# Optimization experiments

Measured on AMD Instinct MI355X. Metric: run time of the kernel, lower is better.

Reference implementation:

```python
import jax, jax.numpy as jnp
import numpy as np

B, S, D = 8, 2048, 512
EPS = 1e-6
ROPE_THETA = 10000.0


def setup_inputs() -> dict:
    key = jax.random.key(0)
    ks = jax.random.split(key, 8)
    scale = 0.02
    return {
        "x": jax.random.normal(ks[0], (B, S, D), dtype=jnp.float32),
        "conv_w": jax.random.normal(ks[1], (D, D, 3), dtype=jnp.float32) * scale,
        "conv_b": jnp.zeros((D,), dtype=jnp.float32),
        "pre_g": jnp.ones((D,), dtype=jnp.float32),
        "q_g": jnp.ones((D,), dtype=jnp.float32),
        "k_g": jnp.ones((D,), dtype=jnp.float32),
        "Wq": jax.random.normal(ks[2], (D, D), dtype=jnp.float32) * scale,
        "Wk": jax.random.normal(ks[3], (D, D), dtype=jnp.float32) * scale,
        "Wv": jax.random.normal(ks[4], (D, D), dtype=jnp.float32) * scale,
    }


def _rmsnorm(x, g, eps=EPS):
    ms = jnp.mean(jnp.square(x), axis=-1, keepdims=True)
    return x * jax.lax.rsqrt(ms + eps) * g


def _rope_tables(seq_len, head_dim, dtype=jnp.float32):
    inv = 1.0 / (ROPE_THETA ** (jnp.arange(0, head_dim, 2, dtype=dtype) / head_dim))
    freqs = jnp.arange(seq_len, dtype=dtype)[:, None] * inv[None, :]  # [S, D/2]
    return jnp.cos(freqs), jnp.sin(freqs)


def _apply_rope(x, cos, sin):
    # x: [B, S, D]; treat last dim as D/2 complex pairs (interleaved real/imag)
    b, s, d = x.shape
    xr = x.reshape(b, s, d // 2, 2)
    x0, x1 = xr[..., 0], xr[..., 1]
    c = cos[None, :, :]
    sn = sin[None, :, :]
    o0 = x0 * c - x1 * sn
    o1 = x0 * sn + x1 * c
    return jnp.stack([o0, o1], axis=-1).reshape(b, s, d)


def reference(x, conv_w, conv_b, pre_g, q_g, k_g, Wq, Wk, Wv):
    b, s, d = x.shape
    # Conv1d over sequence axis (kernel 3, padding 1)
    xc = jnp.transpose(x, (0, 2, 1))  # [B, D, S]
    xc = jax.lax.conv_general_dilated(
        xc, conv_w, window_strides=(1,), padding=[(1, 1)],
        dimension_numbers=("NCH", "OIH", "NCH"))
    xc = xc + conv_b[None, :, None]
    x_norm = _rmsnorm(jnp.transpose(xc, (0, 2, 1)), pre_g)  # [B, S, D]

    q = _rmsnorm(jnp.einsum("bsd,ed->bse", x_norm, Wq), q_g)
    k = _rmsnorm(jnp.einsum("bsd,ed->bse", x_norm, Wk), k_g)
    v = jnp.einsum("bsd,ed->bse", x_norm, Wv)

    cos, sin = _rope_tables(s, d, x.dtype)
    q = _apply_rope(q, cos, sin)
    k = _apply_rope(k, cos, sin)

    scores = jnp.einsum("bqd,bkd->bqk", q, k) / jnp.sqrt(jnp.asarray(d, x.dtype))
    w = jax.nn.softmax(scores, axis=-1)  # dropout is identity in eval mode
    attended = jnp.einsum("bqk,bkd->bqd", w, v)
    out = x + attended
    return out.mean(axis=1)  # [B, D]
```

## Files before the change

### kernel.cpp

```cpp
#include <hip/hip_runtime.h>
#include <math.h>

#define BB 8
#define SS 2048
#define SSG 2050
#define DDIM 512
#define KC 1536
#define EPSV 1e-6f
#define SCALE 0.044194173824159216f

typedef unsigned short ushort_t;
using short8 = __attribute__((ext_vector_type(8))) short;
using f32x4  = __attribute__((ext_vector_type(4))) float;

__device__ inline unsigned short f2bf(float f) {
    union { float f; unsigned int u; } v; v.f = f;
    unsigned int r = v.u + 0x7FFFu + ((v.u >> 16) & 1u);
    return (unsigned short)(r >> 16);
}
__device__ inline unsigned int packbf(float a, float b) {
    return (unsigned int)f2bf(a) | ((unsigned int)f2bf(b) << 16);
}
__device__ inline float bf2f(unsigned short s) {
    union { unsigned int u; float f; } v; v.u = ((unsigned int)s) << 16; return v.f;
}

__device__ inline void gload16(const ushort_t* g, ushort_t* l) {
    __builtin_amdgcn_global_load_lds(
        (__attribute__((address_space(1))) const void*)g,
        (__attribute__((address_space(3))) void*)l, 16, 0, 0);
}

__device__ inline short8 ldswz(const ushort_t* s, int row, int c) {
    return *reinterpret_cast<const short8*>(&s[(row << 6) + ((c ^ (row & 7)) << 3)]);
}

__global__ __launch_bounds__(256) void kx_cast(const float* __restrict__ x,
                                               ushort_t* __restrict__ xbf,
                                               float* __restrict__ xsum)
{
    const int t = threadIdx.x;
    const int b = blockIdx.y;
    const int r0 = blockIdx.x * 16;
    const int c0 = 2 * t;
    if (blockIdx.x == 0) {
        *reinterpret_cast<unsigned int*>(&xbf[((size_t)b * SSG) * DDIM + c0]) = 0u;
        *reinterpret_cast<unsigned int*>(&xbf[((size_t)b * SSG + SS + 1) * DDIM + c0]) = 0u;
    }
    float s0 = 0.f, s1 = 0.f;
    for (int r = 0; r < 16; r++) {
        size_t srow = (size_t)b * SS + r0 + r;
        size_t drow = (size_t)b * SSG + 1 + r0 + r;
        float2 v = *reinterpret_cast<const float2*>(&x[srow * DDIM + c0]);
        s0 += v.x; s1 += v.y;
        *reinterpret_cast<unsigned int*>(&xbf[drow * DDIM + c0]) = packbf(v.x, v.y);
    }
    atomicAdd(&xsum[b * DDIM + c0], s0);
    atomicAdd(&xsum[b * DDIM + c0 + 1], s1);
}

__global__ __launch_bounds__(256) void k0_prep(
    const float* __restrict__ conv_w, const float* __restrict__ Wq,
    const float* __restrict__ Wk, const float* __restrict__ Wv,
    ushort_t* __restrict__ wcat, ushort_t* __restrict__ wqkv)
{
    int idx = blockIdx.x * 256 + threadIdx.x;
    {
        int o = idx / KC, kk = idx - o * KC;
        int t = kk >> 9, i = kk & 511;
        wcat[idx] = f2bf(conv_w[(size_t)o * KC + i * 3 + t]);
    }
    {
        int n = idx >> 9, d = idx & 511;
        const float* src = (n < 512) ? &Wq[(size_t)n * DDIM + d]
                         : (n < 1024) ? &Wk[(size_t)(n - 512) * DDIM + d]
                         : &Wv[(size_t)(n - 1024) * DDIM + d];
        wqkv[idx] = f2bf(*src);
    }
}

#define COMPUTE_TILE(Acur, Bcur) do { \
    _Pragma("unroll") \
    for (int half = 0; half < 2; half++) { \
        const int cb = (half << 2) | lq; \
        short8 af0 = ldswz(Acur, wm * 64 +  0 + lm, cb); \
        short8 af1 = ldswz(Acur, wm * 64 + 16 + lm, cb); \
        short8 af2 = ldswz(Acur, wm * 64 + 32 + lm, cb); \
        short8 af3 = ldswz(Acur, wm * 64 + 48 + lm, cb); \
        _Pragma("unroll") \
        for (int nt = 0; nt < 4; nt++) { \
            short8 bfv = ldswz(Bcur, wn * 64 + nt * 16 + lm, cb); \
            acc[0][nt] = __builtin_amdgcn_mfma_f32_16x16x32_bf16(af0, bfv, acc[0][nt], 0, 0, 0); \
            acc[1][nt] = __builtin_amdgcn_mfma_f32_16x16x32_bf16(af1, bfv, acc[1][nt], 0, 0, 0); \
            acc[2][nt] = __builtin_amdgcn_mfma_f32_16x16x32_bf16(af2, bfv, acc[2][nt], 0, 0, 0); \
            acc[3][nt] = __builtin_amdgcn_mfma_f32_16x16x32_bf16(af3, bfv, acc[3][nt], 0, 0, 0); \
        } \
    } } while (0)

__global__ __launch_bounds__(256) void k1b_conv(
    const ushort_t* __restrict__ xbf, const ushort_t* __restrict__ wcat,
    const float* __restrict__ conv_b, ushort_t* __restrict__ ybf, float* __restrict__ rs)
{
    __shared__ alignas(16) ushort_t As[2][128 * 64];
    __shared__ alignas(16) ushort_t Bs[2][128 * 64];
    const int t = threadIdx.x;
    const int lane = t & 63, w = t >> 6;
    const int lm = lane & 15, lq = lane >> 4;
    const int wm = w >> 1, wn = w & 1;
    const int lr = lane >> 3;
    const int lc = ((lane & 7) ^ lr) << 3;
    const int s0 = blockIdx.x * 128;
    const int n0 = blockIdx.y * 128;
    const int b  = blockIdx.z;
    const ushort_t* Ag = xbf + (size_t)b * SSG * DDIM;
    const ushort_t* Bg = wcat + (size_t)n0 * KC;

    const ushort_t* pa[4]; const ushort_t* pb[4];
    int la[4];
    #pragma unroll
    for (int i = 0; i < 4; i++) {
        const int tr = (w * 4 + i) * 8 + lr;
        pa[i] = &Ag[(size_t)(s0 + tr) * DDIM + lc];
        pb[i] = &Bg[(size_t)tr * KC + lc];
        la[i] = (w * 4 + i) * 512;
    }

    f32x4 acc[4][4];
    #pragma unroll
    for (int i = 0; i < 4; i++)
        #pragma unroll
        for (int j = 0; j < 4; j++) acc[i][j] = (f32x4){0.f, 0.f, 0.f, 0.f};

    #define STG1B(tn, bufi) do { \
        const int koA = (tn) * 64; \
        _Pragma("unroll") \
        for (int i = 0; i < 4; i++) { \
            gload16(pa[i] + koA, &As[bufi][la[i]]); \
            gload16(pb[i] + koA, &Bs[bufi][la[i]]); \
        } } while (0)

    const int NT = 24;
    STG1B(0, 0);
    __syncthreads();
    for (int dc = 0; dc < NT; dc++) {
        const int cur = dc & 1;
        if (dc + 1 < NT) STG1B(dc + 1, cur ^ 1);
        COMPUTE_TILE(&As[cur][0], &Bs[cur][0]);
        __syncthreads();
    }
    #undef STG1B

    const int rbase = s0 + wm * 64;
    const int cbase = n0 + wn * 64;
    ushort_t* yb = ybf + (size_t)b * SS * DDIM;
    float* rsb = rs + (size_t)b * SS;
    float bias[4];
    #pragma unroll
    for (int nt = 0; nt < 4; nt++) bias[nt] = conv_b[cbase + nt * 16 + lm];
    #pragma unroll
    for (int mt = 0; mt < 4; mt++) {
        float pr[4] = {0.f, 0.f, 0.f, 0.f};
        #pragma unroll
        for (int nt = 0; nt < 4; nt++) {
            #pragma unroll
            for (int r = 0; r < 4; r++) {
                float val = acc[mt][nt][r] + bias[nt];
                yb[(size_t)(rbase + mt * 16 + lq * 4 + r) * DDIM + cbase + nt * 16 + lm] = f2bf(val);
                pr[r] = fmaf(val, val, pr[r]);
            }
        }
        #pragma unroll
        for (int r = 0; r < 4; r++) {
            float p = pr[r];
            p += __shfl_xor(p, 1, 64); p += __shfl_xor(p, 2, 64);
            p += __shfl_xor(p, 4, 64); p += __shfl_xor(p, 8, 64);
            if (lm == 0) atomicAdd(&rsb[rbase + mt * 16 + lq * 4 + r], p);
        }
    }
}

__global__ __launch_bounds__(256) void k1n_norm(
    const ushort_t* __restrict__ ybf, const float* __restrict__ rs,
    const float* __restrict__ pre_g, ushort_t* __restrict__ xnbf)
{
    const int t = threadIdx.x;
    const int b = blockIdx.y;
    const int r0 = blockIdx.x * 8;
    float2 pg = *reinterpret_cast<const float2*>(&pre_g[2 * t]);
    for (int r = 0; r < 8; r++) {
        size_t row = (size_t)b * SS + r0 + r;
        float inv = rsqrtf(rs[row] * (1.0f / DDIM) + EPSV);
        unsigned int yv = *reinterpret_cast<const unsigned int*>(&ybf[row * DDIM + 2 * t]);
        float v0 = bf2f((ushort_t)(yv & 0xFFFF)), v1 = bf2f((ushort_t)(yv >> 16));
        *reinterpret_cast<unsigned int*>(&xnbf[row * DDIM + 2 * t]) =
            packbf(v0 * inv * pg.x, v1 * inv * pg.y);
    }
}

__global__ __launch_bounds__(256) void k1c_qkv(
    const ushort_t* __restrict__ xnbf, const ushort_t* __restrict__ wqkv,
    ushort_t* __restrict__ qraw, ushort_t* __restrict__ kraw, ushort_t* __restrict__ vb,
    float* __restrict__ rq, float* __restrict__ rk)
{
    __shared__ alignas(16) ushort_t As[2][128 * 64];
    __shared__ alignas(16) ushort_t Bs[2][128 * 64];
    const int t = threadIdx.x;
    const int lane = t & 63, w = t >> 6;
    const int lm = lane & 15, lq = lane >> 4;
    const int wm = w >> 1, wn = w & 1;
    const int lr = lane >> 3;
    const int lc = ((lane & 7) ^ lr) << 3;
    const int s0 = blockIdx.x * 128;
    const int n0 = blockIdx.y * 128;
    const int b  = blockIdx.z;
    const ushort_t* Ag = xnbf + ((size_t)b * SS + s0) * DDIM;
    const ushort_t* Bg = wqkv + (size_t)n0 * DDIM;

    const ushort_t* pa[4]; const ushort_t* pb[4];
    int la[4];
    #pragma unroll
    for (int i = 0; i < 4; i++) {
        const int tr = (w * 4 + i) * 8 + lr;
        pa[i] = &Ag[(size_t)tr * DDIM + lc];
        pb[i] = &Bg[(size_t)tr * DDIM + lc];
        la[i] = (w * 4 + i) * 512;
    }

    f32x4 acc[4][4];
    #pragma unroll
    for (int i = 0; i < 4; i++)
        #pragma unroll
        for (int j = 0; j < 4; j++) acc[i][j] = (f32x4){0.f, 0.f, 0.f, 0.f};

    #define STG1C(tn, bufi) do { \
        const int ko = (tn) * 64; \
        _Pragma("unroll") \
        for (int i = 0; i < 4; i++) { \
            gload16(pa[i] + ko, &As[bufi][la[i]]); \
            gload16(pb[i] + ko, &Bs[bufi][la[i]]); \
        } } while (0)

    const int NT = 8;
    STG1C(0, 0);
    __syncthreads();
    for (int dc = 0; dc < NT; dc++) {
        const int cur = dc & 1;
        if (dc + 1 < NT) STG1C(dc + 1, cur ^ 1);
        COMPUTE_TILE(&As[cur][0], &Bs[cur][0]);
        __syncthreads();
    }
    #undef STG1C

    const int which = blockIdx.y >> 2;
    const int rbase = s0 + wm * 64;
    const int cbase = ((blockIdx.y & 3) * 128) + wn * 64;
    if (which == 2) {
        ushort_t* vbb = vb + (size_t)b * SS * DDIM;
        #pragma unroll
        for (int mt = 0; mt < 4; mt++)
            #pragma unroll
            for (int nt = 0; nt < 4; nt++)
                #pragma unroll
                for (int r = 0; r < 4; r++)
                    vbb[(size_t)(rbase + mt * 16 + lq * 4 + r) * DDIM + cbase + nt * 16 + lm] =
                        f2bf(acc[mt][nt][r]);
    } else {
        ushort_t* db2 = (which ? kraw : qraw) + (size_t)b * SS * DDIM;
        float* rb = (which ? rk : rq) + (size_t)b * SS;
        #pragma unroll
        for (int mt = 0; mt < 4; mt++) {
            float pr[4] = {0.f, 0.f, 0.f, 0.f};
            #pragma unroll
            for (int nt = 0; nt < 4; nt++) {
                #pragma unroll
                for (int r = 0; r < 4; r++) {
                    float val = acc[mt][nt][r];
                    db2[(size_t)(rbase + mt * 16 + lq * 4 + r) * DDIM + cbase + nt * 16 + lm] = f2bf(val);
                    pr[r] = fmaf(val, val, pr[r]);
                }
            }
            #pragma unroll
            for (int r = 0; r < 4; r++) {
                float p = pr[r];
                p += __shfl_xor(p, 1, 64); p += __shfl_xor(p, 2, 64);
                p += __shfl_xor(p, 4, 64); p += __shfl_xor(p, 8, 64);
                if (lm == 0) atomicAdd(&rb[rbase + mt * 16 + lq * 4 + r], p);
            }
        }
    }
}

__global__ __launch_bounds__(256) void k1d_rope(
    ushort_t* q_io, ushort_t* k_io,
    const float* __restrict__ rq, const float* __restrict__ rk,
    const float* __restrict__ q_g, const float* __restrict__ k_g)
{
    const int t = threadIdx.x;
    const int b = blockIdx.y;
    const int r0 = blockIdx.x * 8;
    const int c0 = 2 * t;
    float qg0 = q_g[c0], qg1 = q_g[c0 + 1];
    float kg0 = k_g[c0], kg1 = k_g[c0 + 1];
    float invf = (float)pow(10000.0, -(double)c0 / (double)DDIM);
    for (int r = 0; r < 8; r++) {
        int srow = r0 + r;
        size_t rowi = (size_t)b * SS + srow;
        float iq = rsqrtf(rq[rowi] * (1.0f / DDIM) + EPSV);
        float ik = rsqrtf(rk[rowi] * (1.0f / DDIM) + EPSV);
        size_t off = rowi * DDIM + c0;
        unsigned int qv = *reinterpret_cast<const unsigned int*>(&q_io[off]);
        unsigned int kv = *reinterpret_cast<const unsigned int*>(&k_io[off]);
        float q0 = bf2f((ushort_t)(qv & 0xFFFF)) * iq * qg0;
        float q1 = bf2f((ushort_t)(qv >> 16)) * iq * qg1;
        float k0v = bf2f((ushort_t)(kv & 0xFFFF)) * ik * kg0;
        float k1v = bf2f((ushort_t)(kv >> 16)) * ik * kg1;
        float ang = (float)srow * invf, sn, cs;
        sincosf(ang, &sn, &cs);
        *reinterpret_cast<unsigned int*>(&q_io[off]) = packbf(q0 * cs - q1 * sn, q0 * sn + q1 * cs);
        *reinterpret_cast<unsigned int*>(&k_io[off]) = packbf(k0v * cs - k1v * sn, k0v * sn + k1v * cs);
    }
}

__global__ __launch_bounds__(256) void k2a_rowsum(
    const ushort_t* __restrict__ qb, const ushort_t* __restrict__ kb,
    ushort_t* __restrict__ P, float* __restrict__ l)
{
    __shared__ alignas(16) ushort_t As[2][128 * 64];
    __shared__ alignas(16) ushort_t Bs[2][128 * 64];
    const int t = threadIdx.x;
    const int lane = t & 63, w = t >> 6;
    const int lm = lane & 15, lq = lane >> 4;
    const int wm = w >> 1, wn = w & 1;
    const int lr = lane >> 3;
    const int lc = ((lane & 7) ^ lr) << 3;
    const int b  = blockIdx.x;
    const int qt = blockIdx.y;
    const int kt = blockIdx.z;
    const ushort_t* Ag = qb + ((size_t)b * SS + qt * 128) * DDIM;
    const ushort_t* Bg = kb + ((size_t)b * SS + kt * 128) * DDIM;

    const ushort_t* pa[4]; const ushort_t* pb[4];
    int la[4];
    #pragma unroll
    for (int i = 0; i < 4; i++) {
        const int tr = (w * 4 + i) * 8 + lr;
        pa[i] = &Ag[(size_t)tr * DDIM + lc];
        pb[i] = &Bg[(size_t)tr * DDIM + lc];
        la[i] = (w * 4 + i) * 512;
    }

    f32x4 acc[4][4];
    #pragma unroll
    for (int i = 0; i < 4; i++)
        #pragma unroll
        for (int j = 0; j < 4; j++) acc[i][j] = (f32x4){0.f, 0.f, 0.f, 0.f};

    #define STG2A(tn, bufi) do { \
        const int ko = (tn) * 64; \
        _Pragma("unroll") \
        for (int i = 0; i < 4; i++) { \
            gload16(pa[i] + ko, &As[bufi][la[i]]); \
            gload16(pb[i] + ko, &Bs[bufi][la[i]]); \
        } } while (0)

    const int NT = 8;
    STG2A(0, 0);
    __syncthreads();
    for (int dc = 0; dc < NT; dc++) {
        const int cur = dc & 1;
        if (dc + 1 < NT) STG2A(dc + 1, cur ^ 1);
        COMPUTE_TILE(&As[cur][0], &Bs[cur][0]);
        __syncthreads();
    }
    #undef STG2A

    const int rbase = qt * 128 + wm * 64;
    const int cbase = kt * 128 + wn * 64;
    ushort_t* Pb = P + (size_t)b * SS * SS;
    float* lrow = l + (size_t)b * SS;
    #pragma unroll
    for (int mt = 0; mt < 4; mt++) {
        #pragma unroll
        for (int r = 0; r < 4; r++) {
            const int row = rbase + mt * 16 + lq * 4 + r;
            float rowp = 0.f;
            #pragma unroll
            for (int nt = 0; nt < 4; nt++) {
                float e = __expf(acc[mt][nt][r] * SCALE);
                Pb[(size_t)row * SS + cbase + nt * 16 + lm] = f2bf(e);
                rowp += e;
            }
            float p = rowp;
            p += __shfl_xor(p, 1, 64); p += __shfl_xor(p, 2, 64);
            p += __shfl_xor(p, 4, 64); p += __shfl_xor(p, 8, 64);
            if (lm == 0) atomicAdd(&lrow[row], p);
        }
    }
}

__global__ __launch_bounds__(256) void k2c_colred(
    const ushort_t* __restrict__ P, const float* __restrict__ l,
    float* __restrict__ cw)
{
    const int t = threadIdx.x;
    const int b = blockIdx.z;
    const int k0 = blockIdx.x * 1024 + t * 4;
    const int q0 = blockIdx.y * 128;
    const ushort_t* Pb = P + ((size_t)b * SS + q0) * SS;
    const float* lb = l + (size_t)b * SS + q0;
    float a0 = 0.f, a1 = 0.f, a2 = 0.f, a3 = 0.f;
    for (int q = 0; q < 128; q++) {
        float rl = 1.0f / lb[q];
        uint2 pp = *reinterpret_cast<const uint2*>(&Pb[(size_t)q * SS + k0]);
        a0 = fmaf(bf2f((ushort_t)(pp.x & 0xFFFF)), rl, a0);
        a1 = fmaf(bf2f((ushort_t)(pp.x >> 16)), rl, a1);
        a2 = fmaf(bf2f((ushort_t)(pp.y & 0xFFFF)), rl, a2);
        a3 = fmaf(bf2f((ushort_t)(pp.y >> 16)), rl, a3);
    }
    atomicAdd(&cw[(size_t)b * SS + k0], a0);
    atomicAdd(&cw[(size_t)b * SS + k0 + 1], a1);
    atomicAdd(&cw[(size_t)b * SS + k0 + 2], a2);
    atomicAdd(&cw[(size_t)b * SS + k0 + 3], a3);
}

__global__ __launch_bounds__(256) void k4_out(
    const float* __restrict__ xsum, const ushort_t* __restrict__ v,
    const float* __restrict__ cwv, float* __restrict__ out)
{
    const int b = blockIdx.x, c = blockIdx.y;
    const int t = threadIdx.x;
    const int srow0 = c * (SS / 16);
    const ushort_t* vb = v + ((size_t)b * SS + srow0) * DDIM;
    const float* cwb   = cwv + (size_t)b * SS + srow0;
    float a0 = (c == 0) ? xsum[b * DDIM + t]       : 0.f;
    float a1 = (c == 0) ? xsum[b * DDIM + t + 256] : 0.f;
    for (int r = 0; r < SS / 16; r++) {
        float w = cwb[r];
        a0 += w * bf2f(vb[(size_t)r * DDIM + t]);
        a1 += w * bf2f(vb[(size_t)r * DDIM + t + 256]);
    }
    atomicAdd(&out[b * DDIM + t],       a0 * (1.0f / SS));
    atomicAdd(&out[b * DDIM + t + 256], a1 * (1.0f / SS));
}

extern "C" void kernel_launch(void* const* d_in, const int* in_sizes, int n_in,
                              void* d_out, int out_size, void* d_ws, size_t ws_size,
                              hipStream_t stream)
{
    const float* x      = (const float*)d_in[0];
    const float* conv_w = (const float*)d_in[1];
    const float* conv_b = (const float*)d_in[2];
    const float* pre_g  = (const float*)d_in[3];
    const float* q_g    = (const float*)d_in[4];
    const float* k_g    = (const float*)d_in[5];
    const float* Wq     = (const float*)d_in[6];
    const float* Wk     = (const float*)d_in[7];
    const float* Wv     = (const float*)d_in[8];
    float* out          = (float*)d_out;

    const size_t NTOK  = (size_t)BB * SS * DDIM;
    const size_t NTOKG = (size_t)BB * SSG * DDIM;
    char* p = (char*)d_ws;
    ushort_t* xbf = (ushort_t*)p; p += NTOKG * 2;
    ushort_t* ybf = (ushort_t*)p; p += NTOK * 2;
    ushort_t* xn  = (ushort_t*)p; p += NTOK * 2;
                         p += NTOK * 2;
    ushort_t* qio = (ushort_t*)p; p += NTOK * 2;
    ushort_t* kio = (ushort_t*)p; p += NTOK * 2;
    ushort_t* vb  = (ushort_t*)p; p += NTOK * 2;
    ushort_t* wcat = (ushort_t*)p; p += (size_t)DDIM * KC * 2;
    ushort_t* wqkv = (ushort_t*)p; p += (size_t)KC * DDIM * 2;
    float* rs   = (float*)p; p += (size_t)BB * SS * 4;
    float* rq   = (float*)p; p += (size_t)BB * SS * 4;
    float* rk   = (float*)p; p += (size_t)BB * SS * 4;
    float* lbuf = (float*)p; p += (size_t)BB * SS * 4;
    float* cwb  = (float*)p; p += (size_t)BB * SS * 4;
    float* xsum = (float*)p; p += (size_t)BB * DDIM * 4;

    ushort_t* Pbuf = xbf;

    (void)hipMemsetAsync(d_out, 0, (size_t)out_size * sizeof(float), stream);
    (void)hipMemsetAsync(rs, 0, ((size_t)BB * SS * 5 + (size_t)BB * DDIM) * sizeof(float), stream);

    kx_cast<<<dim3(SS / 16, BB), 256, 0, stream>>>(x, xbf, xsum);
    k0_prep<<<dim3(DDIM * KC / 256), 256, 0, stream>>>(conv_w, Wq, Wk, Wv, wcat, wqkv);
    k1b_conv<<<dim3(SS / 128, 4, BB), 256, 0, stream>>>(xbf, wcat, conv_b, ybf, rs);
    k1n_norm<<<dim3(SS / 8, BB), 256, 0, stream>>>(ybf, rs, pre_g, xn);
    k1c_qkv<<<dim3(SS / 128, 12, BB), 256, 0, stream>>>(xn, wqkv, qio, kio, vb, rq, rk);
    k1d_rope<<<dim3(SS / 8, BB), 256, 0, stream>>>(qio, kio, rq, rk, q_g, k_g);
    k2a_rowsum<<<dim3(BB, SS / 128, SS / 128), 256, 0, stream>>>(qio, kio, Pbuf, lbuf);
    k2c_colred<<<dim3(SS / 1024, SS / 128, BB), 256, 0, stream>>>(Pbuf, lbuf, cwb);
    k4_out<<<dim3(BB, 16), 256, 0, stream>>>(xsum, vb, cwb, out);
}
```

Measured before the change: 284.0 us.

## Halve GEMM K-tile to 32 with new swizzled LDS layout and precompute RoPE table

```diff
diff --git a/kernel.cpp b/kernel.cpp
--- a/kernel.cpp
+++ b/kernel.cpp
@@ -31,8 +31,10 @@
         (__attribute__((address_space(3))) void*)l, 16, 0, 0);
 }
 
-__device__ inline short8 ldswz(const ushort_t* s, int row, int c) {
-    return *reinterpret_cast<const short8*>(&s[(row << 6) + ((c ^ (row & 7)) << 3)]);
+__device__ inline short8 ldtile(const ushort_t* base, int R, int c) {
+    const int v = R >> 1;
+    const int s = (((c << 1) | (R & 1)) ^ (v & 7));
+    return *reinterpret_cast<const short8*>(&base[v * 64 + s * 8]);
 }
 
 __global__ __launch_bounds__(256) void kx_cast(const float* __restrict__ x,
@@ -79,51 +81,65 @@
     }
 }
 
-#define COMPUTE_TILE(Acur, Bcur) do { \
+__global__ __launch_bounds__(256) void ktab(float* __restrict__ rope)
+{
+    const int t = threadIdx.x;
+    const int r0 = blockIdx.x * 8;
+    const float invf = (float)pow(10000.0, -(double)(2 * t) / (double)DDIM);
+    for (int r = 0; r < 8; r++) {
+        int srow = r0 + r;
+        float sn, cs;
+        sincosf((float)srow * invf, &sn, &cs);
+        *reinterpret_cast<float2*>(&rope[((size_t)srow << 9) + 2 * t]) = make_float2(cs, sn);
+    }
+}
+
+#define COMPUTE_TILE32(Acur, Bcur) do { \
+    short8 av[4], bv[4]; \
     _Pragma("unroll") \
-    for (int half = 0; half < 2; half++) { \
-        const int cb = (half << 2) | lq; \
-        short8 af0 = ldswz(Acur, wm * 64 +  0 + lm, cb); \
-        short8 af1 = ldswz(Acur, wm * 64 + 16 + lm, cb); \
-        short8 af2 = ldswz(Acur, wm * 64 + 32 + lm, cb); \
-        short8 af3 = ldswz(Acur, wm * 64 + 48 + lm, cb); \
+    for (int mt = 0; mt < 4; mt++) av[mt] = ldtile(Acur, wm * 64 + mt * 16 + lm, lq); \
+    _Pragma("unroll") \
+    for (int nt = 0; nt < 4; nt++) bv[nt] = ldtile(Bcur, wn * 64 + nt * 16 + lm, lq); \
+    _Pragma("unroll") \
+    for (int nt = 0; nt < 4; nt++) { \
+        acc[0][nt] = __builtin_amdgcn_mfma_f32_16x16x32_bf16(av[0], bv[nt], acc[0][nt], 0, 0, 0); \
+        acc[1][nt] = __builtin_amdgcn_mfma_f32_16x16x32_bf16(av[1], bv[nt], acc[1][nt], 0, 0, 0); \
+        acc[2][nt] = __builtin_amdgcn_mfma_f32_16x16x32_bf16(av[2], bv[nt], acc[2][nt], 0, 0, 0); \
+        acc[3][nt] = __builtin_amdgcn_mfma_f32_16x16x32_bf16(av[3], bv[nt], acc[3][nt], 0, 0, 0); \
+    } } while (0)
+
+#define STAGE_PTRS(PA, GBASE, PITCH) \
+    { \
         _Pragma("unroll") \
-        for (int nt = 0; nt < 4; nt++) { \
-            short8 bfv = ldswz(Bcur, wn * 64 + nt * 16 + lm, cb); \
-            acc[0][nt] = __builtin_amdgcn_mfma_f32_16x16x32_bf16(af0, bfv, acc[0][nt], 0, 0, 0); \
-            acc[1][nt] = __builtin_amdgcn_mfma_f32_16x16x32_bf16(af1, bfv, acc[1][nt], 0, 0, 0); \
-            acc[2][nt] = __builtin_amdgcn_mfma_f32_16x16x32_bf16(af2, bfv, acc[2][nt], 0, 0, 0); \
-            acc[3][nt] = __builtin_amdgcn_mfma_f32_16x16x32_bf16(af3, bfv, acc[3][nt], 0, 0, 0); \
+        for (int rd = 0; rd < 2; rd++) { \
+            int v = rd * 32 + (t >> 3); \
+            int u = (t & 7) ^ (v & 7); \
+            int lrow = 2 * v + (u & 1); \
+            int chunk = u >> 1; \
+            PA[rd] = &GBASE[(size_t)lrow * (PITCH) + chunk * 8]; \
         } \
-    } } while (0)
+    }
 
 __global__ __launch_bounds__(256) void k1b_conv(
     const ushort_t* __restrict__ xbf, const ushort_t* __restrict__ wcat,
     const float* __restrict__ conv_b, ushort_t* __restrict__ ybf, float* __restrict__ rs)
 {
-    __shared__ alignas(16) ushort_t As[2][128 * 64];
-    __shared__ alignas(16) ushort_t Bs[2][128 * 64];
+    __shared__ alignas(16) ushort_t As[2][4096];
+    __shared__ alignas(16) ushort_t Bs[2][4096];
     const int t = threadIdx.x;
     const int lane = t & 63, w = t >> 6;
     const int lm = lane & 15, lq = lane >> 4;
     const int wm = w >> 1, wn = w & 1;
-    const int lr = lane >> 3;
-    const int lc = ((lane & 7) ^ lr) << 3;
     const int s0 = blockIdx.x * 128;
     const int n0 = blockIdx.y * 128;
     const int b  = blockIdx.z;
-    const ushort_t* Ag = xbf + (size_t)b * SSG * DDIM;
+    const ushort_t* Ag = xbf + ((size_t)b * SSG + s0) * DDIM;
     const ushort_t* Bg = wcat + (size_t)n0 * KC;
 
-    const ushort_t* pa[4]; const ushort_t* pb[4];
-    int la[4];
-    #pragma unroll
-    for (int i = 0; i < 4; i++) {
-        const int tr = (w * 4 + i) * 8 + lr;
-        pa[i] = &Ag[(size_t)(s0 + tr) * DDIM + lc];
-        pb[i] = &Bg[(size_t)tr * KC + lc];
-        la[i] = (w * 4 + i) * 512;
-    }
+    const ushort_t* pa[2]; const ushort_t* pb[2];
+    STAGE_PTRS(pa, Ag, DDIM);
+    STAGE_PTRS(pb, Bg, KC);
+    const int wb = w * 512;
 
     f32x4 acc[4][4];
     #pragma unroll
@@ -131,21 +147,19 @@
         #pragma unroll
         for (int j = 0; j < 4; j++) acc[i][j] = (f32x4){0.f, 0.f, 0.f, 0.f};
 
-    #define STG1B(tn, bufi) do { \
-        const int koA = (tn) * 64; \
-        _Pragma("unroll") \
-        for (int i = 0; i < 4; i++) { \
-            gload16(pa[i] + koA, &As[bufi][la[i]]); \
-            gload16(pb[i] + koA, &Bs[bufi][la[i]]); \
-        } } while (0)
-
-    const int NT = 24;
+    #define STG1B(tn, bufi) do { const int ko = (tn) * 32; \
+        gload16(pa[0] + ko, &As[bufi][wb]); \
+        gload16(pa[1] + ko, &As[bufi][2048 + wb]); \
+        gload16(pb[0] + ko, &Bs[bufi][wb]); \
+        gload16(pb[1] + ko, &Bs[bufi][2048 + wb]); } while (0)
+
+    const int NT = 48;
     STG1B(0, 0);
     __syncthreads();
     for (int dc = 0; dc < NT; dc++) {
         const int cur = dc & 1;
         if (dc + 1 < NT) STG1B(dc + 1, cur ^ 1);
-        COMPUTE_TILE(&As[cur][0], &Bs[cur][0]);
+        COMPUTE_TILE32(&As[cur][0], &Bs[cur][0]);
         __syncthreads();
     }
     #undef STG1B
@@ -202,29 +216,22 @@
     ushort_t* __restrict__ qraw, ushort_t* __restrict__ kraw, ushort_t* __restrict__ vb,
     float* __restrict__ rq, float* __restrict__ rk)
 {
-    __shared__ alignas(16) ushort_t As[2][128 * 64];
-    __shared__ alignas(16) ushort_t Bs[2][128 * 64];
+    __shared__ alignas(16) ushort_t As[2][4096];
+    __shared__ alignas(16) ushort_t Bs[2][4096];
     const int t = threadIdx.x;
     const int lane = t & 63, w = t >> 6;
     const int lm = lane & 15, lq = lane >> 4;
     const int wm = w >> 1, wn = w & 1;
-    const int lr = lane >> 3;
-    const int lc = ((lane & 7) ^ lr) << 3;
     const int s0 = blockIdx.x * 128;
     const int n0 = blockIdx.y * 128;
     const int b  = blockIdx.z;
     const ushort_t* Ag = xnbf + ((size_t)b * SS + s0) * DDIM;
     const ushort_t* Bg = wqkv + (size_t)n0 * DDIM;
 
-    const ushort_t* pa[4]; const ushort_t* pb[4];
-    int la[4];
-    #pragma unroll
-    for (int i = 0; i < 4; i++) {
-        const int tr = (w * 4 + i) * 8 + lr;
-        pa[i] = &Ag[(size_t)tr * DDIM + lc];
-        pb[i] = &Bg[(size_t)tr * DDIM + lc];
-        la[i] = (w * 4 + i) * 512;
-    }
+    const ushort_t* pa[2]; const ushort_t* pb[2];
+    STAGE_PTRS(pa, Ag, DDIM);
+    STAGE_PTRS(pb, Bg, DDIM);
+    const int wb = w * 512;
 
     f32x4 acc[4][4];
     #pragma unroll
@@ -232,21 +239,19 @@
         #pragma unroll
         for (int j = 0; j < 4; j++) acc[i][j] = (f32x4){0.f, 0.f, 0.f, 0.f};
 
-    #define STG1C(tn, bufi) do { \
-        const int ko = (tn) * 64; \
-        _Pragma("unroll") \
-        for (int i = 0; i < 4; i++) { \
-            gload16(pa[i] + ko, &As[bufi][la[i]]); \
-            gload16(pb[i] + ko, &Bs[bufi][la[i]]); \
-        } } while (0)
-
-    const int NT = 8;
+    #define STG1C(tn, bufi) do { const int ko = (tn) * 32; \
+        gload16(pa[0] + ko, &As[bufi][wb]); \
+        gload16(pa[1] + ko, &As[bufi][2048 + wb]); \
+        gload16(pb[0] + ko, &Bs[bufi][wb]); \
+        gload16(pb[1] + ko, &Bs[bufi][2048 + wb]); } while (0)
+
+    const int NT = 16;
     STG1C(0, 0);
     __syncthreads();
     for (int dc = 0; dc < NT; dc++) {
         const int cur = dc & 1;
         if (dc + 1 < NT) STG1C(dc + 1, cur ^ 1);
-        COMPUTE_TILE(&As[cur][0], &Bs[cur][0]);
+        COMPUTE_TILE32(&As[cur][0], &Bs[cur][0]);
         __syncthreads();
     }
     #undef STG1C
@@ -293,7 +298,8 @@
 __global__ __launch_bounds__(256) void k1d_rope(
     ushort_t* q_io, ushort_t* k_io,
     const float* __restrict__ rq, const float* __restrict__ rk,
-    const float* __restrict__ q_g, const float* __restrict__ k_g)
+    const float* __restrict__ q_g, const float* __restrict__ k_g,
+    const float* __restrict__ rope)
 {
     const int t = threadIdx.x;
     const int b = blockIdx.y;
@@ -301,7 +307,6 @@
     const int c0 = 2 * t;
     float qg0 = q_g[c0], qg1 = q_g[c0 + 1];
     float kg0 = k_g[c0], kg1 = k_g[c0 + 1];
-    float invf = (float)pow(10000.0, -(double)c0 / (double)DDIM);
     for (int r = 0; r < 8; r++) {
         int srow = r0 + r;
         size_t rowi = (size_t)b * SS + srow;
@@ -314,8 +319,8 @@
         float q1 = bf2f((ushort_t)(qv >> 16)) * iq * qg1;
         float k0v = bf2f((ushort_t)(kv & 0xFFFF)) * ik * kg0;
         float k1v = bf2f((ushort_t)(kv >> 16)) * ik * kg1;
-        float ang = (float)srow * invf, sn, cs;
-        sincosf(ang, &sn, &cs);
+        float2 cs2 = *reinterpret_cast<const float2*>(&rope[((size_t)srow << 9) + c0]);
+        float cs = cs2.x, sn = cs2.y;
         *reinterpret_cast<unsigned int*>(&q_io[off]) = packbf(q0 * cs - q1 * sn, q0 * sn + q1 * cs);
         *reinterpret_cast<unsigned int*>(&k_io[off]) = packbf(k0v * cs - k1v * sn, k0v * sn + k1v * cs);
     }
@@ -325,29 +330,22 @@
     const ushort_t* __restrict__ qb, const ushort_t* __restrict__ kb,
     ushort_t* __restrict__ P, float* __restrict__ l)
 {
-    __shared__ alignas(16) ushort_t As[2][128 * 64];
-    __shared__ alignas(16) ushort_t Bs[2][128 * 64];
+    __shared__ alignas(16) ushort_t As[2][4096];
+    __shared__ alignas(16) ushort_t Bs[2][4096];
     const int t = threadIdx.x;
     const int lane = t & 63, w = t >> 6;
     const int lm = lane & 15, lq = lane >> 4;
     const int wm = w >> 1, wn = w & 1;
-    const int lr = lane >> 3;
-    const int lc = ((lane & 7) ^ lr) << 3;
     const int b  = blockIdx.x;
     const int qt = blockIdx.y;
     const int kt = blockIdx.z;
     const ushort_t* Ag = qb + ((size_t)b * SS + qt * 128) * DDIM;
     const ushort_t* Bg = kb + ((size_t)b * SS + kt * 128) * DDIM;
 
-    const ushort_t* pa[4]; const ushort_t* pb[4];
-    int la[4];
-    #pragma unroll
-    for (int i = 0; i < 4; i++) {
-        const int tr = (w * 4 + i) * 8 + lr;
-        pa[i] = &Ag[(size_t)tr * DDIM + lc];
-        pb[i] = &Bg[(size_t)tr * DDIM + lc];
-        la[i] = (w * 4 + i) * 512;
-    }
+    const ushort_t* pa[2]; const ushort_t* pb[2];
+    STAGE_PTRS(pa, Ag, DDIM);
+    STAGE_PTRS(pb, Bg, DDIM);
+    const int wb = w * 512;
 
     f32x4 acc[4][4];
     #pragma unroll
@@ -355,21 +353,19 @@
         #pragma unroll
         for (int j = 0; j < 4; j++) acc[i][j] = (f32x4){0.f, 0.f, 0.f, 0.f};
 
-    #define STG2A(tn, bufi) do { \
-        const int ko = (tn) * 64; \
-        _Pragma("unroll") \
-        for (int i = 0; i < 4; i++) { \
-            gload16(pa[i] + ko, &As[bufi][la[i]]); \
-            gload16(pb[i] + ko, &Bs[bufi][la[i]]); \
-        } } while (0)
-
-    const int NT = 8;
+    #define STG2A(tn, bufi) do { const int ko = (tn) * 32; \
+        gload16(pa[0] + ko, &As[bufi][wb]); \
+        gload16(pa[1] + ko, &As[bufi][2048 + wb]); \
+        gload16(pb[0] + ko, &Bs[bufi][wb]); \
+        gload16(pb[1] + ko, &Bs[bufi][2048 + wb]); } while (0)
+
+    const int NT = 16;
     STG2A(0, 0);
     __syncthreads();
     for (int dc = 0; dc < NT; dc++) {
         const int cur = dc & 1;
         if (dc + 1 < NT) STG2A(dc + 1, cur ^ 1);
-        COMPUTE_TILE(&As[cur][0], &Bs[cur][0]);
+        COMPUTE_TILE32(&As[cur][0], &Bs[cur][0]);
         __syncthreads();
     }
     #undef STG2A
@@ -464,7 +460,7 @@
     ushort_t* xbf = (ushort_t*)p; p += NTOKG * 2;
     ushort_t* ybf = (ushort_t*)p; p += NTOK * 2;
     ushort_t* xn  = (ushort_t*)p; p += NTOK * 2;
-                         p += NTOK * 2;
+    char* padreg = p;             p += NTOK * 2;
     ushort_t* qio = (ushort_t*)p; p += NTOK * 2;
     ushort_t* kio = (ushort_t*)p; p += NTOK * 2;
     ushort_t* vb  = (ushort_t*)p; p += NTOK * 2;
@@ -478,16 +474,18 @@
     float* xsum = (float*)p; p += (size_t)BB * DDIM * 4;
 
     ushort_t* Pbuf = xbf;
+    float* rope = (float*)padreg;
 
     (void)hipMemsetAsync(d_out, 0, (size_t)out_size * sizeof(float), stream);
     (void)hipMemsetAsync(rs, 0, ((size_t)BB * SS * 5 + (size_t)BB * DDIM) * sizeof(float), stream);
 
     kx_cast<<<dim3(SS / 16, BB), 256, 0, stream>>>(x, xbf, xsum);
     k0_prep<<<dim3(DDIM * KC / 256), 256, 0, stream>>>(conv_w, Wq, Wk, Wv, wcat, wqkv);
+    ktab<<<dim3(SS / 8), 256, 0, stream>>>(rope);
     k1b_conv<<<dim3(SS / 128, 4, BB), 256, 0, stream>>>(xbf, wcat, conv_b, ybf, rs);
     k1n_norm<<<dim3(SS / 8, BB), 256, 0, stream>>>(ybf, rs, pre_g, xn);
     k1c_qkv<<<dim3(SS / 128, 12, BB), 256, 0, stream>>>(xn, wqkv, qio, kio, vb, rq, rk);
-    k1d_rope<<<dim3(SS / 8, BB), 256, 0, stream>>>(qio, kio, rq, rk, q_g, k_g);
+    k1d_rope<<<dim3(SS / 8, BB), 256, 0, stream>>>(qio, kio, rq, rk, q_g, k_g, rope);
     k2a_rowsum<<<dim3(BB, SS / 128, SS / 128), 256, 0, stream>>>(qio, kio, Pbuf, lbuf);
     k2c_colred<<<dim3(SS / 1024, SS / 128, BB), 256, 0, stream>>>(Pbuf, lbuf, cwb);
     k4_out<<<dim3(BB, 16), 256, 0, stream>>>(xsum, vb, cwb, out);
```

New measurement: 291.3 us. +2.5%, slower.

## Stage GEMM epilogues through LDS for wide stores, single-buffer tiles, precompute RoPE table

Applied to the files above, without the earlier changes.

```diff
diff --git a/kernel.cpp b/kernel.cpp
--- a/kernel.cpp
+++ b/kernel.cpp
@@ -35,6 +35,10 @@
     return *reinterpret_cast<const short8*>(&s[(row << 6) + ((c ^ (row & 7)) << 3)]);
 }
 
+__device__ inline ushort_t* crow_ptr(ushort_t* As, ushort_t* Bs, int row) {
+    return row < 64 ? As + row * 128 : Bs + (row - 64) * 128;
+}
+
 __global__ __launch_bounds__(256) void kx_cast(const float* __restrict__ x,
                                                ushort_t* __restrict__ xbf,
                                                float* __restrict__ xsum)
@@ -76,6 +80,19 @@
                          : (n < 1024) ? &Wk[(size_t)(n - 512) * DDIM + d]
                          : &Wv[(size_t)(n - 1024) * DDIM + d];
         wqkv[idx] = f2bf(*src);
+    }
+}
+
+__global__ __launch_bounds__(256) void ktab(float* __restrict__ rope)
+{
+    const int t = threadIdx.x;
+    const int r0 = blockIdx.x * 8;
+    const float invf = (float)pow(10000.0, -(double)(2 * t) / (double)DDIM);
+    for (int r = 0; r < 8; r++) {
+        int srow = r0 + r;
+        float sn, cs;
+        sincosf((float)srow * invf, &sn, &cs);
+        *reinterpret_cast<float2*>(&rope[((size_t)srow << 9) + 2 * t]) = make_float2(cs, sn);
     }
 }
 
@@ -97,12 +114,23 @@
         } \
     } } while (0)
 
+#define CSTORE_WIDE(GDSTROW, GPITCH) do { \
+    const int row_l = t >> 1, half_ = t & 1, r7_ = row_l & 7; \
+    const ushort_t* src_ = crow_ptr(As, Bs, row_l); \
+    ushort_t* gdst_ = (GDSTROW); \
+    _Pragma("unroll") \
+    for (int i = 0; i < 8; i++) { \
+        const int j = half_ * 8 + i; \
+        *reinterpret_cast<short8*>(&gdst_[j * 8]) = \
+            *reinterpret_cast<const short8*>(&src_[(j ^ r7_) << 3]); \
+    } } while (0)
+
 __global__ __launch_bounds__(256) void k1b_conv(
     const ushort_t* __restrict__ xbf, const ushort_t* __restrict__ wcat,
     const float* __restrict__ conv_b, ushort_t* __restrict__ ybf, float* __restrict__ rs)
 {
-    __shared__ alignas(16) ushort_t As[2][128 * 64];
-    __shared__ alignas(16) ushort_t Bs[2][128 * 64];
+    __shared__ alignas(16) ushort_t As[128 * 64];
+    __shared__ alignas(16) ushort_t Bs[128 * 64];
     const int t = threadIdx.x;
     const int lane = t & 63, w = t >> 6;
     const int lm = lane & 15, lq = lane >> 4;
@@ -131,52 +159,48 @@
         #pragma unroll
         for (int j = 0; j < 4; j++) acc[i][j] = (f32x4){0.f, 0.f, 0.f, 0.f};
 
-    #define STG1B(tn, bufi) do { \
-        const int koA = (tn) * 64; \
-        _Pragma("unroll") \
-        for (int i = 0; i < 4; i++) { \
-            gload16(pa[i] + koA, &As[bufi][la[i]]); \
-            gload16(pb[i] + koA, &Bs[bufi][la[i]]); \
-        } } while (0)
-
-    const int NT = 24;
-    STG1B(0, 0);
-    __syncthreads();
-    for (int dc = 0; dc < NT; dc++) {
-        const int cur = dc & 1;
-        if (dc + 1 < NT) STG1B(dc + 1, cur ^ 1);
-        COMPUTE_TILE(&As[cur][0], &Bs[cur][0]);
-        __syncthreads();
-    }
-    #undef STG1B
+    for (int dc = 0; dc < 24; dc++) {
+        __syncthreads();
+        const int koff = dc * 64;
+        #pragma unroll
+        for (int i = 0; i < 4; i++) {
+            gload16(pa[i] + koff, &As[la[i]]);
+            gload16(pb[i] + koff, &Bs[la[i]]);
+        }
+        __syncthreads();
+        COMPUTE_TILE(As, Bs);
+    }
 
     const int rbase = s0 + wm * 64;
     const int cbase = n0 + wn * 64;
-    ushort_t* yb = ybf + (size_t)b * SS * DDIM;
     float* rsb = rs + (size_t)b * SS;
     float bias[4];
     #pragma unroll
     for (int nt = 0; nt < 4; nt++) bias[nt] = conv_b[cbase + nt * 16 + lm];
+    __syncthreads();
     #pragma unroll
     for (int mt = 0; mt < 4; mt++) {
-        float pr[4] = {0.f, 0.f, 0.f, 0.f};
-        #pragma unroll
-        for (int nt = 0; nt < 4; nt++) {
+        #pragma unroll
+        for (int r = 0; r < 4; r++) {
+            const int rl = wm * 64 + mt * 16 + lq * 4 + r;
+            ushort_t* lr_p = crow_ptr(As, Bs, rl);
+            const int r7 = rl & 7;
+            float pr = 0.f;
             #pragma unroll
-            for (int r = 0; r < 4; r++) {
+            for (int nt = 0; nt < 4; nt++) {
                 float val = acc[mt][nt][r] + bias[nt];
-                yb[(size_t)(rbase + mt * 16 + lq * 4 + r) * DDIM + cbase + nt * 16 + lm] = f2bf(val);
-                pr[r] = fmaf(val, val, pr[r]);
+                const int c = wn * 64 + nt * 16 + lm;
+                lr_p[(((c >> 3) ^ r7) << 3) | (c & 7)] = f2bf(val);
+                pr = fmaf(val, val, pr);
             }
-        }
-        #pragma unroll
-        for (int r = 0; r < 4; r++) {
-            float p = pr[r];
-            p += __shfl_xor(p, 1, 64); p += __shfl_xor(p, 2, 64);
-            p += __shfl_xor(p, 4, 64); p += __shfl_xor(p, 8, 64);
-            if (lm == 0) atomicAdd(&rsb[rbase + mt * 16 + lq * 4 + r], p);
-        }
-    }
+            pr += __shfl_xor(pr, 1, 64); pr += __shfl_xor(pr, 2, 64);
+            pr += __shfl_xor(pr, 4, 64); pr += __shfl_xor(pr, 8, 64);
+            if (lm == 0) atomicAdd(&rsb[rbase + mt * 16 + lq * 4 + r], pr);
+        }
+    }
+    __syncthreads();
+    ushort_t* yb = ybf + (size_t)b * SS * DDIM;
+    CSTORE_WIDE(&yb[(size_t)(s0 + (t >> 1)) * DDIM + n0], DDIM);
 }
 
 __global__ __launch_bounds__(256) void k1n_norm(
@@ -202,8 +226,8 @@
     ushort_t* __restrict__ qraw, ushort_t* __restrict__ kraw, ushort_t* __restrict__ vb,
     float* __restrict__ rq, float* __restrict__ rk)
 {
-    __shared__ alignas(16) ushort_t As[2][128 * 64];
-    __shared__ alignas(16) ushort_t Bs[2][128 * 64];
+    __shared__ alignas(16) ushort_t As[128 * 64];
+    __shared__ alignas(16) ushort_t Bs[128 * 64];
     const int t = threadIdx.x;
     const int lane = t & 63, w = t >> 6;
     const int lm = lane & 15, lq = lane >> 4;
@@ -232,68 +256,73 @@
         #pragma unroll
         for (int j = 0; j < 4; j++) acc[i][j] = (f32x4){0.f, 0.f, 0.f, 0.f};
 
-    #define STG1C(tn, bufi) do { \
-        const int ko = (tn) * 64; \
-        _Pragma("unroll") \
-        for (int i = 0; i < 4; i++) { \
-            gload16(pa[i] + ko, &As[bufi][la[i]]); \
-            gload16(pb[i] + ko, &Bs[bufi][la[i]]); \
-        } } while (0)
-
-    const int NT = 8;
-    STG1C(0, 0);
-    __syncthreads();
-    for (int dc = 0; dc < NT; dc++) {
-        const int cur = dc & 1;
-        if (dc + 1 < NT) STG1C(dc + 1, cur ^ 1);
-        COMPUTE_TILE(&As[cur][0], &Bs[cur][0]);
-        __syncthreads();
-    }
-    #undef STG1C
+    for (int dc = 0; dc < 8; dc++) {
+        __syncthreads();
+        const int koff = dc * 64;
+        #pragma unroll
+        for (int i = 0; i < 4; i++) {
+            gload16(pa[i] + koff, &As[la[i]]);
+            gload16(pb[i] + koff, &Bs[la[i]]);
+        }
+        __syncthreads();
+        COMPUTE_TILE(As, Bs);
+    }
 
     const int which = blockIdx.y >> 2;
     const int rbase = s0 + wm * 64;
-    const int cbase = ((blockIdx.y & 3) * 128) + wn * 64;
+    const int gc0   = (blockIdx.y & 3) * 128;
+    __syncthreads();
     if (which == 2) {
-        ushort_t* vbb = vb + (size_t)b * SS * DDIM;
-        #pragma unroll
-        for (int mt = 0; mt < 4; mt++)
+        #pragma unroll
+        for (int mt = 0; mt < 4; mt++) {
             #pragma unroll
-            for (int nt = 0; nt < 4; nt++)
+            for (int r = 0; r < 4; r++) {
+                const int rl = wm * 64 + mt * 16 + lq * 4 + r;
+                ushort_t* lr_p = crow_ptr(As, Bs, rl);
+                const int r7 = rl & 7;
                 #pragma unroll
-                for (int r = 0; r < 4; r++)
-                    vbb[(size_t)(rbase + mt * 16 + lq * 4 + r) * DDIM + cbase + nt * 16 + lm] =
-                        f2bf(acc[mt][nt][r]);
-    } else {
-        ushort_t* db2 = (which ? kraw : qraw) + (size_t)b * SS * DDIM;
-        float* rb = (which ? rk : rq) + (size_t)b * SS;
-        #pragma unroll
-        for (int mt = 0; mt < 4; mt++) {
-            float pr[4] = {0.f, 0.f, 0.f, 0.f};
-            #pragma unroll
-            for (int nt = 0; nt < 4; nt++) {
-                #pragma unroll
-                for (int r = 0; r < 4; r++) {
-                    float val = acc[mt][nt][r];
-                    db2[(size_t)(rbase + mt * 16 + lq * 4 + r) * DDIM + cbase + nt * 16 + lm] = f2bf(val);
-                    pr[r] = fmaf(val, val, pr[r]);
+                for (int nt = 0; nt < 4; nt++) {
+                    const int c = wn * 64 + nt * 16 + lm;
+                    lr_p[(((c >> 3) ^ r7) << 3) | (c & 7)] = f2bf(acc[mt][nt][r]);
                 }
             }
+        }
+        __syncthreads();
+        ushort_t* vbb = vb + (size_t)b * SS * DDIM;
+        CSTORE_WIDE(&vbb[(size_t)(s0 + (t >> 1)) * DDIM + gc0], DDIM);
+    } else {
+        float* rb = (which ? rk : rq) + (size_t)b * SS;
+        #pragma unroll
+        for (int mt = 0; mt < 4; mt++) {
             #pragma unroll
             for (int r = 0; r < 4; r++) {
-                float p = pr[r];
-                p += __shfl_xor(p, 1, 64); p += __shfl_xor(p, 2, 64);
-                p += __shfl_xor(p, 4, 64); p += __shfl_xor(p, 8, 64);
-                if (lm == 0) atomicAdd(&rb[rbase + mt * 16 + lq * 4 + r], p);
+                const int rl = wm * 64 + mt * 16 + lq * 4 + r;
+                ushort_t* lr_p = crow_ptr(As, Bs, rl);
+                const int r7 = rl & 7;
+                float pr = 0.f;
+                #pragma unroll
+                for (int nt = 0; nt < 4; nt++) {
+                    float val = acc[mt][nt][r];
+                    const int c = wn * 64 + nt * 16 + lm;
+                    lr_p[(((c >> 3) ^ r7) << 3) | (c & 7)] = f2bf(val);
+                    pr = fmaf(val, val, pr);
+                }
+                pr += __shfl_xor(pr, 1, 64); pr += __shfl_xor(pr, 2, 64);
+                pr += __shfl_xor(pr, 4, 64); pr += __shfl_xor(pr, 8, 64);
+                if (lm == 0) atomicAdd(&rb[rbase + mt * 16 + lq * 4 + r], pr);
             }
         }
+        __syncthreads();
+        ushort_t* db2 = (which ? kraw : qraw) + (size_t)b * SS * DDIM;
+        CSTORE_WIDE(&db2[(size_t)(s0 + (t >> 1)) * DDIM + gc0], DDIM);
     }
 }
 
 __global__ __launch_bounds__(256) void k1d_rope(
     ushort_t* q_io, ushort_t* k_io,
     const float* __restrict__ rq, const float* __restrict__ rk,
-    const float* __restrict__ q_g, const float* __restrict__ k_g)
+    const float* __restrict__ q_g, const float* __restrict__ k_g,
+    const float* __restrict__ rope)
 {
     const int t = threadIdx.x;
     const int b = blockIdx.y;
@@ -301,7 +330,6 @@
     const int c0 = 2 * t;
     float qg0 = q_g[c0], qg1 = q_g[c0 + 1];
     float kg0 = k_g[c0], kg1 = k_g[c0 + 1];
-    float invf = (float)pow(10000.0, -(double)c0 / (double)DDIM);
     for (int r = 0; r < 8; r++) {
         int srow = r0 + r;
         size_t rowi = (size_t)b * SS + srow;
@@ -314,8 +342,8 @@
         float q1 = bf2f((ushort_t)(qv >> 16)) * iq * qg1;
         float k0v = bf2f((ushort_t)(kv & 0xFFFF)) * ik * kg0;
         float k1v = bf2f((ushort_t)(kv >> 16)) * ik * kg1;
-        float ang = (float)srow * invf, sn, cs;
-        sincosf(ang, &sn, &cs);
+        float2 cs2 = *reinterpret_cast<const float2*>(&rope[((size_t)srow << 9) + c0]);
+        float cs = cs2.x, sn = cs2.y;
         *reinterpret_cast<unsigned int*>(&q_io[off]) = packbf(q0 * cs - q1 * sn, q0 * sn + q1 * cs);
         *reinterpret_cast<unsigned int*>(&k_io[off]) = packbf(k0v * cs - k1v * sn, k0v * sn + k1v * cs);
     }
@@ -325,8 +353,8 @@
     const ushort_t* __restrict__ qb, const ushort_t* __restrict__ kb,
     ushort_t* __restrict__ P, float* __restrict__ l)
 {
-    __shared__ alignas(16) ushort_t As[2][128 * 64];
-    __shared__ alignas(16) ushort_t Bs[2][128 * 64];
+    __shared__ alignas(16) ushort_t As[128 * 64];
+    __shared__ alignas(16) ushort_t Bs[128 * 64];
     const int t = threadIdx.x;
     const int lane = t & 63, w = t >> 6;
     const int lm = lane & 15, lq = lane >> 4;
@@ -355,47 +383,43 @@
         #pragma unroll
         for (int j = 0; j < 4; j++) acc[i][j] = (f32x4){0.f, 0.f, 0.f, 0.f};
 
-    #define STG2A(tn, bufi) do { \
-        const int ko = (tn) * 64; \
-        _Pragma("unroll") \
-        for (int i = 0; i < 4; i++) { \
-            gload16(pa[i] + ko, &As[bufi][la[i]]); \
-            gload16(pb[i] + ko, &Bs[bufi][la[i]]); \
-        } } while (0)
-
-    const int NT = 8;
-    STG2A(0, 0);
+    for (int dc = 0; dc < 8; dc++) {
+        __syncthreads();
+        const int koff = dc * 64;
+        #pragma unroll
+        for (int i = 0; i < 4; i++) {
+            gload16(pa[i] + koff, &As[la[i]]);
+            gload16(pb[i] + koff, &Bs[la[i]]);
+        }
+        __syncthreads();
+        COMPUTE_TILE(As, Bs);
+    }
+
+    float* lrow = l + (size_t)b * SS + qt * 128;
     __syncthreads();
-    for (int dc = 0; dc < NT; dc++) {
-        const int cur = dc & 1;
-        if (dc + 1 < NT) STG2A(dc + 1, cur ^ 1);
-        COMPUTE_TILE(&As[cur][0], &Bs[cur][0]);
-        __syncthreads();
-    }
-    #undef STG2A
-
-    const int rbase = qt * 128 + wm * 64;
-    const int cbase = kt * 128 + wn * 64;
-    ushort_t* Pb = P + (size_t)b * SS * SS;
-    float* lrow = l + (size_t)b * SS;
     #pragma unroll
     for (int mt = 0; mt < 4; mt++) {
         #pragma unroll
         for (int r = 0; r < 4; r++) {
-            const int row = rbase + mt * 16 + lq * 4 + r;
+            const int rl = wm * 64 + mt * 16 + lq * 4 + r;
+            ushort_t* lr_p = crow_ptr(As, Bs, rl);
+            const int r7 = rl & 7;
             float rowp = 0.f;
             #pragma unroll
             for (int nt = 0; nt < 4; nt++) {
                 float e = __expf(acc[mt][nt][r] * SCALE);
-                Pb[(size_t)row * SS + cbase + nt * 16 + lm] = f2bf(e);
+                const int c = wn * 64 + nt * 16 + lm;
+                lr_p[(((c >> 3) ^ r7) << 3) | (c & 7)] = f2bf(e);
                 rowp += e;
             }
-            float p = rowp;
-            p += __shfl_xor(p, 1, 64); p += __shfl_xor(p, 2, 64);
-            p += __shfl_xor(p, 4, 64); p += __shfl_xor(p, 8, 64);
-            if (lm == 0) atomicAdd(&lrow[row], p);
-        }
-    }
+            rowp += __shfl_xor(rowp, 1, 64); rowp += __shfl_xor(rowp, 2, 64);
+            rowp += __shfl_xor(rowp, 4, 64); rowp += __shfl_xor(rowp, 8, 64);
+            if (lm == 0) atomicAdd(&lrow[rl], rowp);
+        }
+    }
+    __syncthreads();
+    ushort_t* Pb = P + (size_t)b * SS * SS;
+    CSTORE_WIDE(&Pb[(size_t)(qt * 128 + (t >> 1)) * SS + kt * 128], SS);
 }
 
 __global__ __launch_bounds__(256) void k2c_colred(
@@ -464,7 +488,7 @@
     ushort_t* xbf = (ushort_t*)p; p += NTOKG * 2;
     ushort_t* ybf = (ushort_t*)p; p += NTOK * 2;
     ushort_t* xn  = (ushort_t*)p; p += NTOK * 2;
-                         p += NTOK * 2;
+    char* padreg = p;             p += NTOK * 2;
     ushort_t* qio = (ushort_t*)p; p += NTOK * 2;
     ushort_t* kio = (ushort_t*)p; p += NTOK * 2;
     ushort_t* vb  = (ushort_t*)p; p += NTOK * 2;
@@ -478,16 +502,18 @@
     float* xsum = (float*)p; p += (size_t)BB * DDIM * 4;
 
     ushort_t* Pbuf = xbf;
+    float* rope = (float*)padreg;
 
     (void)hipMemsetAsync(d_out, 0, (size_t)out_size * sizeof(float), stream);
     (void)hipMemsetAsync(rs, 0, ((size_t)BB * SS * 5 + (size_t)BB * DDIM) * sizeof(float), stream);
 
     kx_cast<<<dim3(SS / 16, BB), 256, 0, stream>>>(x, xbf, xsum);
     k0_prep<<<dim3(DDIM * KC / 256), 256, 0, stream>>>(conv_w, Wq, Wk, Wv, wcat, wqkv);
+    ktab<<<dim3(SS / 8), 256, 0, stream>>>(rope);
     k1b_conv<<<dim3(SS / 128, 4, BB), 256, 0, stream>>>(xbf, wcat, conv_b, ybf, rs);
     k1n_norm<<<dim3(SS / 8, BB), 256, 0, stream>>>(ybf, rs, pre_g, xn);
     k1c_qkv<<<dim3(SS / 128, 12, BB), 256, 0, stream>>>(xn, wqkv, qio, kio, vb, rq, rk);
-    k1d_rope<<<dim3(SS / 8, BB), 256, 0, stream>>>(qio, kio, rq, rk, q_g, k_g);
+    k1d_rope<<<dim3(SS / 8, BB), 256, 0, stream>>>(qio, kio, rq, rk, q_g, k_g, rope);
     k2a_rowsum<<<dim3(BB, SS / 128, SS / 128), 256, 0, stream>>>(qio, kio, Pbuf, lbuf);
     k2c_colred<<<dim3(SS / 1024, SS / 128, BB), 256, 0, stream>>>(Pbuf, lbuf, cwb);
     k4_out<<<dim3(BB, 16), 256, 0, stream>>>(xsum, vb, cwb, out);
```

After: 314.4 us. +10.7%, slower.
